# Performance work log

Measured on AMD Instinct MI355X. Metric: run time of the kernel, lower is better.

The kernel has to match this reference:

```python
import jax, jax.numpy as jnp
import numpy as np

NUM_HEADS = 16


def setup_inputs() -> dict:
    key = jax.random.key(0)
    ks = jax.random.split(key, 5)
    B, L, D = 2, 2048, 1024
    x = jax.random.normal(ks[0], (B, L, D), dtype=jnp.float32)
    s = 1.0 / np.sqrt(D)
    Wqkv_w = jax.random.normal(ks[1], (3 * D, D), dtype=jnp.float32) * s
    Wqkv_b = jax.random.normal(ks[2], (3 * D,), dtype=jnp.float32) * 0.01
    out_w = jax.random.normal(ks[3], (D, D), dtype=jnp.float32) * s
    out_b = jax.random.normal(ks[4], (D,), dtype=jnp.float32) * 0.01
    return {"x": x, "Wqkv_w": Wqkv_w, "Wqkv_b": Wqkv_b, "out_w": out_w, "out_b": out_b}


def reference(x, Wqkv_w, Wqkv_b, out_w, out_b):
    B, L, D = x.shape
    H = NUM_HEADS
    d = D // H
    scale = 1.0 / np.sqrt(d).astype(np.float32)
    # qkv projection: torch Linear is x @ W^T + b
    qkv = x @ Wqkv_w.T + Wqkv_b                      # [B, L, 3D]
    qkv = qkv.reshape(B, L, 3, H, d)                 # (three h d) split
    qkv = jnp.transpose(qkv, (2, 0, 3, 1, 4))        # [3, B, H, L, d]
    q, k, v = qkv[0], qkv[1], qkv[2]
    k = k * scale
    # Linear-attention recurrence S_t = S_{t-1} + v_t k_t^T, y_t = S_t q_t
    # == causally-masked unnormalized attention: y_t = sum_{s<=t} (q_t.k_s) v_s
    scores = jnp.einsum('bhld,bhmd->bhlm', q, k)     # [B,H,L,L]
    causal = jnp.tril(jnp.ones((L, L), dtype=scores.dtype))
    y = jnp.einsum('bhlm,bhmd->bhld', scores * causal, v)  # [B,H,L,d]
    y = jnp.transpose(y, (0, 2, 1, 3)).reshape(B, L, D)    # b l (h d)
    return y @ out_w.T + out_b
```

## Files before the change

### kernel.cpp

```cpp
#include <hip/hip_runtime.h>


#define DEV __device__ __forceinline__

typedef __attribute__((ext_vector_type(8))) short bf16x8;
typedef __attribute__((ext_vector_type(4))) float f32x4;

DEV ushort f2bf(float f) {
  union { float f; unsigned u; } v; v.f = f;
  unsigned r = v.u + 0x7fffu + ((v.u >> 16) & 1u);
  return (ushort)(r >> 16);
}
DEV float bf2f(unsigned b) {
  union { unsigned u; float f; } v; v.u = (b & 0xffffu) << 16;
  return v.f;
}
DEV void glds16(const ushort* g, ushort* l) {
  __builtin_amdgcn_global_load_lds(
      (const __attribute__((address_space(1))) unsigned int*)g,
      (__attribute__((address_space(3))) unsigned int*)l, 16, 0, 0);
}

__global__ __launch_bounds__(256) void cvt_all(const float* __restrict__ x,
                                               const float* __restrict__ Ww,
                                               const float* __restrict__ Ow,
                                               ushort* __restrict__ xb,
                                               ushort* __restrict__ wqkvb,
                                               ushort* __restrict__ outwb) {
  int i = blockIdx.x * 256 + threadIdx.x;
  const float* src; ushort* dst; int off;
  if (i < 1048576)      { src = x;  dst = xb;    off = i; }
  else if (i < 1835008) { src = Ww; dst = wqkvb; off = i - 1048576; }
  else                  { src = Ow; dst = outwb; off = i - 1835008; }
  float4 v = ((const float4*)src)[off];
  ushort4 o;
  o.x = f2bf(v.x); o.y = f2bf(v.y); o.z = f2bf(v.z); o.w = f2bf(v.w);
  ((ushort4*)dst)[off] = o;
}

template <bool OUT_BF16, bool KSCALE>
__global__ __launch_bounds__(256) void gemm_bt(const ushort* __restrict__ A,
                                               const ushort* __restrict__ Bw,
                                               const float* __restrict__ bias,
                                               void* __restrict__ Cout,
                                               int M, int N, int K) {
  __shared__ ushort As[128 * 32];
  __shared__ ushort Bs[128 * 32];
  const int t = threadIdx.x;
  const int wid = t >> 6, lane = t & 63;
  const int quad = lane >> 4, l16 = lane & 15;
  const int bm = blockIdx.y * 128, bn = blockIdx.x * 128;
  const int wm = (wid >> 1) * 64, wn = (wid & 1) * 64;

  f32x4 acc[4][4];
  const f32x4 z = {0.f, 0.f, 0.f, 0.f};
#pragma unroll
  for (int i = 0; i < 4; ++i)
#pragma unroll
    for (int j = 0; j < 4; ++j) acc[i][j] = z;

  const int sl = lane ^ ((lane >> 3) & 7);
  const ushort* ag = A + (size_t)(bm + wid * 16 + (sl >> 2)) * K + ((sl & 3) * 8);
  const ushort* bg = Bw + (size_t)(bn + wid * 16 + (sl >> 2)) * K + ((sl & 3) * 8);
  ushort* asl = As + wid * 512;
  ushort* bsl = Bs + wid * 512;
  const size_t rowskip = (size_t)64 * K;

  const int rslot = ((l16 * 4 + quad) ^ (l16 >> 1)) * 8;

  for (int k0 = 0; k0 < K; k0 += 32) {
    glds16(ag + k0, asl);
    glds16(ag + k0 + rowskip, asl + 2048);
    glds16(bg + k0, bsl);
    glds16(bg + k0 + rowskip, bsl + 2048);
    __syncthreads();
    bf16x8 af[4], bf[4];
#pragma unroll
    for (int i = 0; i < 4; ++i) {
      af[i] = *(const bf16x8*)(As + ((wm >> 4) + i) * 512 + rslot);
      bf[i] = *(const bf16x8*)(Bs + ((wn >> 4) + i) * 512 + rslot);
    }
#pragma unroll
    for (int i = 0; i < 4; ++i)
#pragma unroll
      for (int j = 0; j < 4; ++j)
        acc[i][j] = __builtin_amdgcn_mfma_f32_16x16x32_bf16(af[i], bf[j], acc[i][j], 0, 0, 0);
    __syncthreads();
  }

#pragma unroll
  for (int i = 0; i < 4; ++i)
#pragma unroll
    for (int j = 0; j < 4; ++j) {
      const int col = bn + wn + j * 16 + l16;
      const float bv = bias[col];
      float sc = 1.f;
      if (KSCALE) sc = ((col >> 10) == 1) ? 0.125f : 1.f;
#pragma unroll
      for (int r = 0; r < 4; ++r) {
        const int row = bm + wm + i * 16 + quad * 4 + r;
        const float v = (acc[i][j][r] + bv) * sc;
        if (OUT_BF16)
          ((ushort*)Cout)[(size_t)row * N + col] = f2bf(v);
        else
          ((float*)Cout)[(size_t)row * N + col] = v;
      }
    }
}

__global__ __launch_bounds__(256) void gemm_out64(const ushort* __restrict__ A,
                                                  const ushort* __restrict__ Bw,
                                                  const float* __restrict__ bias,
                                                  float* __restrict__ C,
                                                  int M, int N, int K) {
  __shared__ ushort As[64 * 32];
  __shared__ ushort Bs[128 * 32];
  const int t = threadIdx.x;
  const int wid = t >> 6, lane = t & 63;
  const int quad = lane >> 4, l16 = lane & 15;
  const int bm = blockIdx.y * 64, bn = blockIdx.x * 128;
  const int wn = wid * 32;

  f32x4 acc[4][2];
  const f32x4 z = {0.f, 0.f, 0.f, 0.f};
#pragma unroll
  for (int i = 0; i < 4; ++i) { acc[i][0] = z; acc[i][1] = z; }

  const int sl = lane ^ ((lane >> 3) & 7);
  const ushort* ag = A + (size_t)(bm + wid * 16 + (sl >> 2)) * K + ((sl & 3) * 8);
  const ushort* bg = Bw + (size_t)(bn + wid * 16 + (sl >> 2)) * K + ((sl & 3) * 8);
  ushort* asl = As + wid * 512;
  ushort* bsl = Bs + wid * 512;
  const size_t rowskip = (size_t)64 * K;
  const int rslot = ((l16 * 4 + quad) ^ (l16 >> 1)) * 8;

  for (int k0 = 0; k0 < K; k0 += 32) {
    glds16(ag + k0, asl);
    glds16(bg + k0, bsl);
    glds16(bg + k0 + rowskip, bsl + 2048);
    __syncthreads();
    bf16x8 af[4], bf[2];
#pragma unroll
    for (int i = 0; i < 4; ++i)
      af[i] = *(const bf16x8*)(As + i * 512 + rslot);
#pragma unroll
    for (int j = 0; j < 2; ++j)
      bf[j] = *(const bf16x8*)(Bs + (wid * 2 + j) * 512 + rslot);
#pragma unroll
    for (int i = 0; i < 4; ++i)
#pragma unroll
      for (int j = 0; j < 2; ++j)
        acc[i][j] = __builtin_amdgcn_mfma_f32_16x16x32_bf16(af[i], bf[j], acc[i][j], 0, 0, 0);
    __syncthreads();
  }

#pragma unroll
  for (int i = 0; i < 4; ++i)
#pragma unroll
    for (int j = 0; j < 2; ++j) {
      const int col = bn + wn + j * 16 + l16;
      const float bv = bias[col];
#pragma unroll
      for (int r = 0; r < 4; ++r) {
        const int row = bm + i * 16 + quad * 4 + r;
        C[(size_t)row * N + col] = acc[i][j][r] + bv;
      }
    }
}

__global__ __launch_bounds__(256) void kv_local(const ushort* __restrict__ qkv,
                                                float* __restrict__ mlocT) {
  const int c = blockIdx.x, bh = blockIdx.y;
  const int b = bh >> 4, hd = bh & 15;
  const int t = threadIdx.x;
  __shared__ float kk[32 * 65];
  __shared__ float vv[32 * 65];
  float s[16];
#pragma unroll
  for (int j = 0; j < 16; ++j) s[j] = 0.f;
  const int e = t >> 2, fb = (t & 3) * 16;
  const int step = t >> 3, el = (t & 7) * 8;
  for (int sb = 0; sb < 4; ++sb) {
    const ushort* kg = qkv + (size_t)(b * 2048 + c * 128 + sb * 32 + step) * 3072 + 1024 + hd * 64 + el;
    uint4 kr = *(const uint4*)kg;
    uint4 vr = *(const uint4*)(kg + 1024);
    float* kd = kk + step * 65 + el;
    float* vd = vv + step * 65 + el;
    kd[0] = bf2f(kr.x); kd[1] = bf2f(kr.x >> 16);
    kd[2] = bf2f(kr.y); kd[3] = bf2f(kr.y >> 16);
    kd[4] = bf2f(kr.z); kd[5] = bf2f(kr.z >> 16);
    kd[6] = bf2f(kr.w); kd[7] = bf2f(kr.w >> 16);
    vd[0] = bf2f(vr.x); vd[1] = bf2f(vr.x >> 16);
    vd[2] = bf2f(vr.y); vd[3] = bf2f(vr.y >> 16);
    vd[4] = bf2f(vr.z); vd[5] = bf2f(vr.z >> 16);
    vd[6] = bf2f(vr.w); vd[7] = bf2f(vr.w >> 16);
    __syncthreads();
    for (int l = 0; l < 32; ++l) {
      const float ve = vv[l * 65 + e];
      const float* krow = kk + l * 65 + fb;
#pragma unroll
      for (int j = 0; j < 16; ++j) s[j] += ve * krow[j];
    }
    __syncthreads();
  }
  float* out = mlocT + ((size_t)bh * 16 + c) * 4096 + e * 64 + fb;
#pragma unroll
  for (int j = 0; j < 16; ++j) out[j] = s[j];
}

__global__ __launch_bounds__(256) void attn_chunk(const ushort* __restrict__ qkv,
                                                  const float* __restrict__ mlocT,
                                                  ushort* __restrict__ yb) {
  const int c = blockIdx.x, bh = blockIdx.y;
  const int b = bh >> 4, hd = bh & 15;
  const int l0 = c * 128;
  const int t = threadIdx.x;
  const int wid = t >> 6, lane = t & 63;
  const int quad = lane >> 4, l16 = lane & 15;

  __shared__ ushort P[16384];
  __shared__ ushort U[16384];
  ushort* Qs = U;
  ushort* Ks = U + 8192;
  ushort* vT = U;
  ushort* sT = U + 8704;

  {
    uint4 zz; zz.x = zz.y = zz.z = zz.w = 0u;
    uint4* p4 = (uint4*)P;
#pragma unroll
    for (int i = 0; i < 8; ++i) p4[i * 256 + t] = zz;
  }
  {
    const int kcs = ((lane & 7) ^ (lane >> 3)) * 8;
    const ushort* qg = qkv + (size_t)(b * 2048 + l0 + (t >> 3)) * 3072 + hd * 64 + kcs;
    ushort* ql = Qs + wid * 512;
    ushort* kl = Ks + wid * 512;
#pragma unroll
    for (int h2 = 0; h2 < 4; ++h2) {
      glds16(qg + (size_t)h2 * 32 * 3072, ql + h2 * 2048);
      glds16(qg + (size_t)h2 * 32 * 3072 + 1024, kl + h2 * 2048);
    }
  }

  float run[16];
#pragma unroll
  for (int j = 0; j < 16; ++j) run[j] = 0.f;
  {
    const float4* mb = (const float4*)mlocT + (size_t)bh * 16384 + (size_t)t * 4;
    for (int cp = 0; cp < c; ++cp) {
      const float4* mc = mb + (size_t)cp * 1024;
#pragma unroll
      for (int k = 0; k < 4; ++k) {
        const float4 m = mc[k];
        run[k * 4 + 0] += m.x; run[k * 4 + 1] += m.y;
        run[k * 4 + 2] += m.z; run[k * 4 + 3] += m.w;
      }
    }
  }
  __syncthreads();

  bf16x8 qf[2][2];
#pragma unroll
  for (int i = 0; i < 2; ++i)
#pragma unroll
    for (int kc = 0; kc < 2; ++kc)
      qf[i][kc] = *(const bf16x8*)(Qs + ((wid * 2 + i) * 16 + l16) * 64 +
                                   (((kc * 4 + quad) ^ (l16 & 7)) * 8));

  const f32x4 z4 = {0.f, 0.f, 0.f, 0.f};
  f32x4 pacc[2][8];
#pragma unroll
  for (int i = 0; i < 2; ++i)
#pragma unroll
    for (int j = 0; j < 8; ++j) pacc[i][j] = z4;

#pragma unroll
  for (int i = 0; i < 2; ++i) {
    const int rt = wid * 2 + i;
#pragma unroll
    for (int tj = 0; tj < 8; ++tj) {
      if (tj <= rt) {
#pragma unroll
        for (int kc = 0; kc < 2; ++kc) {
          bf16x8 kfr = *(const bf16x8*)(Ks + (tj * 16 + l16) * 64 +
                                        (((kc * 4 + quad) ^ (l16 & 7)) * 8));
          pacc[i][tj] = __builtin_amdgcn_mfma_f32_16x16x32_bf16(qf[i][kc], kfr, pacc[i][tj], 0, 0, 0);
        }
      }
    }
  }
  __syncthreads();

#pragma unroll
  for (int i = 0; i < 2; ++i) {
    const int rt = wid * 2 + i;
#pragma unroll
    for (int tj = 0; tj < 8; ++tj) {
      if (tj <= rt) {
#pragma unroll
        for (int r = 0; r < 4; ++r) {
          const int row = rt * 16 + quad * 4 + r;
          const int scol = tj * 16 + l16;
          const float v = (scol <= row) ? pacc[i][tj][r] : 0.f;
          P[row * 128 + (((scol >> 3) ^ (row & 7)) * 8) + (scol & 7)] = f2bf(v);
        }
      }
    }
  }
  {
    const int sstep = t >> 1, eb = (t & 1) * 32;
    const ushort* vg = qkv + (size_t)(b * 2048 + l0 + sstep) * 3072 + 2048 + hd * 64 + eb;
    ushort tmp[32];
    *(uint4*)(tmp + 0)  = *(const uint4*)(vg + 0);
    *(uint4*)(tmp + 8)  = *(const uint4*)(vg + 8);
    *(uint4*)(tmp + 16) = *(const uint4*)(vg + 16);
    *(uint4*)(tmp + 24) = *(const uint4*)(vg + 24);
#pragma unroll
    for (int j = 0; j < 32; ++j) vT[(eb + j) * 136 + sstep] = tmp[j];
  }
  {
#pragma unroll
    for (int j = 0; j < 16; ++j) {
      const int ef = t * 16 + j;
      sT[(ef >> 6) * 72 + (ef & 63)] = f2bf(run[j]);
    }
  }
  __syncthreads();

  f32x4 yacc[2][4];
#pragma unroll
  for (int i = 0; i < 2; ++i)
#pragma unroll
    for (int j = 0; j < 4; ++j) yacc[i][j] = z4;

#pragma unroll
  for (int i = 0; i < 2; ++i) {
    const int rt = wid * 2 + i;
    const int kcmax = rt >> 1;
#pragma unroll
    for (int kc = 0; kc < 4; ++kc) {
      if (kc <= kcmax) {
        const int prow = rt * 16 + l16;
        bf16x8 pf;
        *(uint4*)&pf = *(const uint4*)(P + prow * 128 + (((kc * 4 + quad) ^ (prow & 7)) * 8));
#pragma unroll
        for (int ct = 0; ct < 4; ++ct) {
          bf16x8 vf = *(const bf16x8*)(vT + (ct * 16 + l16) * 136 + kc * 32 + quad * 8);
          yacc[i][ct] = __builtin_amdgcn_mfma_f32_16x16x32_bf16(pf, vf, yacc[i][ct], 0, 0, 0);
        }
      }
    }
#pragma unroll
    for (int kc = 0; kc < 2; ++kc) {
#pragma unroll
      for (int ct = 0; ct < 4; ++ct) {
        bf16x8 sf = *(const bf16x8*)(sT + (ct * 16 + l16) * 72 + kc * 32 + quad * 8);
        yacc[i][ct] = __builtin_amdgcn_mfma_f32_16x16x32_bf16(qf[i][kc], sf, yacc[i][ct], 0, 0, 0);
      }
    }
  }

#pragma unroll
  for (int i = 0; i < 2; ++i) {
    const int rt = wid * 2 + i;
#pragma unroll
    for (int ct = 0; ct < 4; ++ct) {
#pragma unroll
      for (int r = 0; r < 4; ++r) {
        const int row = rt * 16 + quad * 4 + r;
        const int e = ct * 16 + l16;
        yb[(size_t)(b * 2048 + l0 + row) * 1024 + hd * 64 + e] = f2bf(yacc[i][ct][r]);
      }
    }
  }
}

extern "C" void kernel_launch(void* const* d_in, const int* in_sizes, int n_in,
                              void* d_out, int out_size, void* d_ws, size_t ws_size,
                              hipStream_t stream) {
  const float* x  = (const float*)d_in[0];
  const float* Ww = (const float*)d_in[1];
  const float* Wb = (const float*)d_in[2];
  const float* Ow = (const float*)d_in[3];
  const float* Ob = (const float*)d_in[4];
  float* out = (float*)d_out;

  char* ws = (char*)d_ws;
  ushort* xb    = (ushort*)(ws);
  ushort* wqkvb = (ushort*)(ws + (size_t)8  * 1024 * 1024);
  ushort* outwb = (ushort*)(ws + (size_t)14 * 1024 * 1024);
  ushort* qkvb  = (ushort*)(ws + (size_t)16 * 1024 * 1024);
  float*  mlocT = (float*) (ws + (size_t)40 * 1024 * 1024);
  ushort* yb    = (ushort*)(ws + (size_t)48 * 1024 * 1024);

  cvt_all<<<8192, 256, 0, stream>>>(x, Ww, Ow, xb, wqkvb, outwb);
  gemm_bt<true, true><<<dim3(24, 32), 256, 0, stream>>>(xb, wqkvb, Wb, (void*)qkvb, 4096, 3072, 1024);
  kv_local<<<dim3(16, 32), 256, 0, stream>>>(qkvb, mlocT);
  attn_chunk<<<dim3(16, 32), 256, 0, stream>>>(qkvb, mlocT, yb);
  gemm_out64<<<dim3(8, 64), 256, 0, stream>>>(yb, outwb, Ob, out, 4096, 1024, 1024);
}
```

Before: 190.1 us.

## Compute kv_local chunk states with MFMA and drop GEMM LDS swizzle

```diff
diff --git a/kernel.cpp b/kernel.cpp
--- a/kernel.cpp
+++ b/kernel.cpp
@@ -59,14 +59,11 @@
 #pragma unroll
     for (int j = 0; j < 4; ++j) acc[i][j] = z;
 
-  const int sl = lane ^ ((lane >> 3) & 7);
-  const ushort* ag = A + (size_t)(bm + wid * 16 + (sl >> 2)) * K + ((sl & 3) * 8);
-  const ushort* bg = Bw + (size_t)(bn + wid * 16 + (sl >> 2)) * K + ((sl & 3) * 8);
+  const ushort* ag = A + (size_t)(bm + (t >> 2)) * K + ((t & 3) * 8);
+  const ushort* bg = Bw + (size_t)(bn + (t >> 2)) * K + ((t & 3) * 8);
   ushort* asl = As + wid * 512;
   ushort* bsl = Bs + wid * 512;
   const size_t rowskip = (size_t)64 * K;
-
-  const int rslot = ((l16 * 4 + quad) ^ (l16 >> 1)) * 8;
 
   for (int k0 = 0; k0 < K; k0 += 32) {
     glds16(ag + k0, asl);
@@ -77,8 +74,8 @@
     bf16x8 af[4], bf[4];
 #pragma unroll
     for (int i = 0; i < 4; ++i) {
-      af[i] = *(const bf16x8*)(As + ((wm >> 4) + i) * 512 + rslot);
-      bf[i] = *(const bf16x8*)(Bs + ((wn >> 4) + i) * 512 + rslot);
+      af[i] = *(const bf16x8*)(As + (wm + i * 16 + l16) * 32 + quad * 8);
+      bf[i] = *(const bf16x8*)(Bs + (wn + i * 16 + l16) * 32 + quad * 8);
     }
 #pragma unroll
     for (int i = 0; i < 4; ++i)
@@ -126,13 +123,11 @@
 #pragma unroll
   for (int i = 0; i < 4; ++i) { acc[i][0] = z; acc[i][1] = z; }
 
-  const int sl = lane ^ ((lane >> 3) & 7);
-  const ushort* ag = A + (size_t)(bm + wid * 16 + (sl >> 2)) * K + ((sl & 3) * 8);
-  const ushort* bg = Bw + (size_t)(bn + wid * 16 + (sl >> 2)) * K + ((sl & 3) * 8);
+  const ushort* ag = A + (size_t)(bm + (t >> 2)) * K + ((t & 3) * 8);
+  const ushort* bg = Bw + (size_t)(bn + (t >> 2)) * K + ((t & 3) * 8);
   ushort* asl = As + wid * 512;
   ushort* bsl = Bs + wid * 512;
   const size_t rowskip = (size_t)64 * K;
-  const int rslot = ((l16 * 4 + quad) ^ (l16 >> 1)) * 8;
 
   for (int k0 = 0; k0 < K; k0 += 32) {
     glds16(ag + k0, asl);
@@ -142,10 +137,10 @@
     bf16x8 af[4], bf[2];
 #pragma unroll
     for (int i = 0; i < 4; ++i)
-      af[i] = *(const bf16x8*)(As + i * 512 + rslot);
+      af[i] = *(const bf16x8*)(As + (i * 16 + l16) * 32 + quad * 8);
 #pragma unroll
     for (int j = 0; j < 2; ++j)
-      bf[j] = *(const bf16x8*)(Bs + (wid * 2 + j) * 512 + rslot);
+      bf[j] = *(const bf16x8*)(Bs + (wn + j * 16 + l16) * 32 + quad * 8);
 #pragma unroll
     for (int i = 0; i < 4; ++i)
 #pragma unroll
@@ -173,39 +168,45 @@
   const int c = blockIdx.x, bh = blockIdx.y;
   const int b = bh >> 4, hd = bh & 15;
   const int t = threadIdx.x;
-  __shared__ float kk[32 * 65];
-  __shared__ float vv[32 * 65];
-  float s[16];
-#pragma unroll
-  for (int j = 0; j < 16; ++j) s[j] = 0.f;
-  const int e = t >> 2, fb = (t & 3) * 16;
-  const int step = t >> 3, el = (t & 7) * 8;
-  for (int sb = 0; sb < 4; ++sb) {
-    const ushort* kg = qkv + (size_t)(b * 2048 + c * 128 + sb * 32 + step) * 3072 + 1024 + hd * 64 + el;
-    uint4 kr = *(const uint4*)kg;
-    uint4 vr = *(const uint4*)(kg + 1024);
-    float* kd = kk + step * 65 + el;
-    float* vd = vv + step * 65 + el;
-    kd[0] = bf2f(kr.x); kd[1] = bf2f(kr.x >> 16);
-    kd[2] = bf2f(kr.y); kd[3] = bf2f(kr.y >> 16);
-    kd[4] = bf2f(kr.z); kd[5] = bf2f(kr.z >> 16);
-    kd[6] = bf2f(kr.w); kd[7] = bf2f(kr.w >> 16);
-    vd[0] = bf2f(vr.x); vd[1] = bf2f(vr.x >> 16);
-    vd[2] = bf2f(vr.y); vd[3] = bf2f(vr.y >> 16);
-    vd[4] = bf2f(vr.z); vd[5] = bf2f(vr.z >> 16);
-    vd[6] = bf2f(vr.w); vd[7] = bf2f(vr.w >> 16);
-    __syncthreads();
-    for (int l = 0; l < 32; ++l) {
-      const float ve = vv[l * 65 + e];
-      const float* krow = kk + l * 65 + fb;
-#pragma unroll
-      for (int j = 0; j < 16; ++j) s[j] += ve * krow[j];
-    }
-    __syncthreads();
-  }
-  float* out = mlocT + ((size_t)bh * 16 + c) * 4096 + e * 64 + fb;
-#pragma unroll
-  for (int j = 0; j < 16; ++j) out[j] = s[j];
+  const int wid = t >> 6, lane = t & 63;
+  const int quad = lane >> 4, l16 = lane & 15;
+  __shared__ ushort kT[64 * 136];
+  __shared__ ushort vT[64 * 136];
+
+  {
+    const int row = t & 127;
+    const int isv = t >> 7;
+    const ushort* g = qkv + (size_t)(b * 2048 + c * 128 + row) * 3072 +
+                      1024 + isv * 1024 + hd * 64;
+    ushort tmp[64];
+#pragma unroll
+    for (int q = 0; q < 8; ++q) *(uint4*)(tmp + q * 8) = *(const uint4*)(g + q * 8);
+    ushort* dst = isv ? vT : kT;
+#pragma unroll
+    for (int j = 0; j < 64; ++j) dst[j * 136 + row] = tmp[j];
+  }
+  __syncthreads();
+
+  const f32x4 z = {0.f, 0.f, 0.f, 0.f};
+  f32x4 acc[4];
+#pragma unroll
+  for (int ct = 0; ct < 4; ++ct) acc[ct] = z;
+#pragma unroll
+  for (int kc = 0; kc < 4; ++kc) {
+    bf16x8 afr = *(const bf16x8*)(vT + (wid * 16 + l16) * 136 + kc * 32 + quad * 8);
+#pragma unroll
+    for (int ct = 0; ct < 4; ++ct) {
+      bf16x8 bfr = *(const bf16x8*)(kT + (ct * 16 + l16) * 136 + kc * 32 + quad * 8);
+      acc[ct] = __builtin_amdgcn_mfma_f32_16x16x32_bf16(afr, bfr, acc[ct], 0, 0, 0);
+    }
+  }
+
+  float* outp = mlocT + ((size_t)bh * 16 + c) * 4096;
+#pragma unroll
+  for (int ct = 0; ct < 4; ++ct)
+#pragma unroll
+    for (int r = 0; r < 4; ++r)
+      outp[(wid * 16 + quad * 4 + r) * 64 + ct * 16 + l16] = acc[ct][r];
 }
 
 __global__ __launch_bounds__(256) void attn_chunk(const ushort* __restrict__ qkv,
```

Measured after the change: 170.4 us. -10.3%, faster.
